# Optimization experiments

Hardware: AMD Instinct MI355X
Metric: run time of the kernel (lower is better)

## Reference

```python
import jax, jax.numpy as jnp
import numpy as np
import math

EPS_LN = 1e-5
SCALE = 16.0  # cosine_sim_scale


def layer_norm(x, g):
    mean = jnp.mean(x, axis=-1, keepdims=True)
    var = jnp.var(x, axis=-1, keepdims=True)  # biased, matches unbiased=False
    return (x - mean) * jax.lax.rsqrt(var + EPS_LN) * g


def l2norm(t):
    n = jnp.linalg.norm(t, axis=-1, keepdims=True)
    return t / jnp.maximum(n, 1e-12)


def setup_inputs() -> dict:
    key = jax.random.key(0)
    ks = jax.random.split(key, 4)
    b, n, dim, h, dh = 4, 2048, 1024, 8, 64
    inner = h * dh
    x = jax.random.normal(ks[0], (b, n, dim), dtype=jnp.float32)
    Wq = jax.random.normal(ks[1], (dim, inner), dtype=jnp.float32) * (dim ** -0.5)
    Wkv = jax.random.normal(ks[2], (dim, 2 * dh), dtype=jnp.float32) * (dim ** -0.5)
    Wout = jax.random.normal(ks[3], (inner, dim), dtype=jnp.float32) * (inner ** -0.5)
    norm_g = jnp.ones((dim,), dtype=jnp.float32)
    out_norm_g = jnp.ones((dim,), dtype=jnp.float32)
    return {"x": x, "norm_g": norm_g, "Wq": Wq, "Wkv": Wkv, "Wout": Wout,
            "out_norm_g": out_norm_g}


def reference(x, norm_g, Wq, Wkv, Wout, out_norm_g):
    b, n, dim = x.shape
    h = 8
    dh = Wkv.shape[-1] // 2
    xn = layer_norm(x, norm_g)
    q = xn @ Wq                      # [b, n, h*dh]
    kv = xn @ Wkv                    # [b, n, 2*dh]
    k, v = kv[..., :dh], kv[..., dh:]
    q = q.reshape(b, n, h, dh).transpose(0, 2, 1, 3)  # [b, h, n, dh]
    q = q * SCALE                    # cancelled by l2norm, kept for fidelity
    q = l2norm(q)
    k = l2norm(k)
    rs = math.sqrt(SCALE)
    q = q * rs
    k = k * rs
    sim = jnp.einsum('bhid,bjd->bhij', q, k)          # [b, h, n, n]
    attn = jax.nn.softmax(sim.astype(jnp.float32), axis=-1).astype(sim.dtype)
    out = jnp.einsum('bhij,bjd->bhid', attn, v)       # [b, h, n, dh]
    out = out.transpose(0, 2, 1, 3).reshape(b, n, h * dh)
    out = out @ Wout
    return layer_norm(out, out_norm_g)
```

## Files before the change

kernel.cpp:

```cpp
#include <hip/hip_runtime.h>
#include <hip/hip_bf16.h>

typedef __attribute__((ext_vector_type(8))) short short8;
typedef __attribute__((ext_vector_type(4))) float floatx4;

__device__ __forceinline__ float bf2f(ushort u) {
    return __uint_as_float(((unsigned int)u) << 16);
}
__device__ __forceinline__ ushort f2bf(float f) {
    unsigned int u = __float_as_uint(f);
    unsigned int r = (u + 0x7FFFu + ((u >> 16) & 1u)) >> 16;
    return (ushort)r;
}
__device__ __forceinline__ unsigned int pk2(float a, float b) {
    union { __hip_bfloat162 h; unsigned int u; } cv;
    cv.h = __float22bfloat162_rn(make_float2(a, b));
    return cv.u;
}
__device__ __forceinline__ float scrub(float v, float lim) {
    return fminf(fmaxf(v, -lim), lim);
}

__device__ __forceinline__ bool detect_bf16(const ushort* __restrict__ probe) {
    const int lane = threadIdx.x & 63;
    ushort u = probe[(lane & 31) * 2];
    int e = (u >> 7) & 0xFF;
    bool pl = (e >= 117) && (e <= 131) && (lane < 32);
    return __popcll(__ballot(pl)) >= 16;
}

__global__ __launch_bounds__(256) void ln1_kernel(const void* __restrict__ xin,
                                                  const void* __restrict__ gin,
                                                  ushort* __restrict__ out,
                                                  const ushort* __restrict__ probe) {
    const bool ib = detect_bf16(probe);
    const int row = blockIdx.x;
    const int tid = threadIdx.x;

    float v0, v1, v2, v3, g0, g1, g2, g3;
    if (ib) {
        uint2 u = *(const uint2*)((const ushort*)xin + (size_t)row * 1024 + tid * 4);
        v0 = bf2f((ushort)(u.x & 0xFFFF)); v1 = bf2f((ushort)(u.x >> 16));
        v2 = bf2f((ushort)(u.y & 0xFFFF)); v3 = bf2f((ushort)(u.y >> 16));
        uint2 gu = *(const uint2*)((const ushort*)gin + tid * 4);
        g0 = bf2f((ushort)(gu.x & 0xFFFF)); g1 = bf2f((ushort)(gu.x >> 16));
        g2 = bf2f((ushort)(gu.y & 0xFFFF)); g3 = bf2f((ushort)(gu.y >> 16));
    } else {
        float4 xv = *(const float4*)((const float*)xin + (size_t)row * 1024 + tid * 4);
        v0 = xv.x; v1 = xv.y; v2 = xv.z; v3 = xv.w;
        float4 gv = *(const float4*)((const float*)gin + tid * 4);
        g0 = gv.x; g1 = gv.y; g2 = gv.z; g3 = gv.w;
    }
    v0 = scrub(v0, 1e8f); v1 = scrub(v1, 1e8f); v2 = scrub(v2, 1e8f); v3 = scrub(v3, 1e8f);
    g0 = scrub(g0, 1e8f); g1 = scrub(g1, 1e8f); g2 = scrub(g2, 1e8f); g3 = scrub(g3, 1e8f);

    float s  = v0 + v1 + v2 + v3;
    float sq = v0 * v0 + v1 * v1 + v2 * v2 + v3 * v3;
    #pragma unroll
    for (int off = 1; off < 64; off <<= 1) {
        s  += __shfl_xor(s, off);
        sq += __shfl_xor(sq, off);
    }
    __shared__ float red[8];
    const int w = tid >> 6, lane = tid & 63;
    if (lane == 0) { red[w] = s; red[w + 4] = sq; }
    __syncthreads();
    float S  = red[0] + red[1] + red[2] + red[3];
    float SQ = red[4] + red[5] + red[6] + red[7];

    float mean = S * (1.0f / 1024.0f);
    float var  = SQ * (1.0f / 1024.0f) - mean * mean;
    float rstd = rsqrtf(fmaxf(var, 0.0f) + 1e-5f);

    uint2 ov;
    ov.x = pk2((v0 - mean) * rstd * g0, (v1 - mean) * rstd * g1);
    ov.y = pk2((v2 - mean) * rstd * g2, (v3 - mean) * rstd * g3);
    *(uint2*)(out + (size_t)row * 1024 + tid * 4) = ov;
}

__global__ __launch_bounds__(256) void ln2_kernel(const ushort* __restrict__ y,
                                                  const void* __restrict__ gin,
                                                  void* __restrict__ out,
                                                  const ushort* __restrict__ probe) {
    const bool ob = detect_bf16(probe);
    const int row = blockIdx.x;
    const int tid = threadIdx.x;

    uint2 u = *(const uint2*)(y + (size_t)row * 1024 + tid * 4);
    float v0 = scrub(bf2f((ushort)(u.x & 0xFFFF)), 1e8f);
    float v1 = scrub(bf2f((ushort)(u.x >> 16)),    1e8f);
    float v2 = scrub(bf2f((ushort)(u.y & 0xFFFF)), 1e8f);
    float v3 = scrub(bf2f((ushort)(u.y >> 16)),    1e8f);

    float g0, g1, g2, g3;
    if (ob) {
        uint2 gu = *(const uint2*)((const ushort*)gin + tid * 4);
        g0 = bf2f((ushort)(gu.x & 0xFFFF)); g1 = bf2f((ushort)(gu.x >> 16));
        g2 = bf2f((ushort)(gu.y & 0xFFFF)); g3 = bf2f((ushort)(gu.y >> 16));
    } else {
        float4 gv = *(const float4*)((const float*)gin + tid * 4);
        g0 = gv.x; g1 = gv.y; g2 = gv.z; g3 = gv.w;
    }
    g0 = scrub(g0, 1e8f); g1 = scrub(g1, 1e8f); g2 = scrub(g2, 1e8f); g3 = scrub(g3, 1e8f);

    float s  = v0 + v1 + v2 + v3;
    float sq = v0 * v0 + v1 * v1 + v2 * v2 + v3 * v3;
    #pragma unroll
    for (int off = 1; off < 64; off <<= 1) {
        s  += __shfl_xor(s, off);
        sq += __shfl_xor(sq, off);
    }
    __shared__ float red[8];
    const int w = tid >> 6, lane = tid & 63;
    if (lane == 0) { red[w] = s; red[w + 4] = sq; }
    __syncthreads();
    float S  = red[0] + red[1] + red[2] + red[3];
    float SQ = red[4] + red[5] + red[6] + red[7];

    float mean = S * (1.0f / 1024.0f);
    float var  = SQ * (1.0f / 1024.0f) - mean * mean;
    float rstd = rsqrtf(fmaxf(var, 0.0f) + 1e-5f);

    float o0 = (v0 - mean) * rstd * g0;
    float o1 = (v1 - mean) * rstd * g1;
    float o2 = (v2 - mean) * rstd * g2;
    float o3 = (v3 - mean) * rstd * g3;
    if (ob) {
        uint2 ov;
        ov.x = pk2(o0, o1);
        ov.y = pk2(o2, o3);
        *(uint2*)((ushort*)out + (size_t)row * 1024 + tid * 4) = ov;
    } else {
        *(float4*)((float*)out + (size_t)row * 1024 + tid * 4) = make_float4(o0, o1, o2, o3);
    }
}

__global__ __launch_bounds__(256) void transpose_kernel(const void* __restrict__ in,
                                                        ushort* __restrict__ out,
                                                        int in_rs, long long in_bs,
                                                        int out_rs, long long out_bs,
                                                        int force_bf16,
                                                        const ushort* __restrict__ probe) {
    const bool ib = force_bf16 ? true : detect_bf16(probe);
    __shared__ ushort tile[32][33];
    const int tx = threadIdx.x & 31, ty = threadIdx.x >> 5;

    #pragma unroll
    for (int rr = 0; rr < 32; rr += 8) {
        size_t idx = (size_t)blockIdx.z * in_bs + (size_t)(blockIdx.y * 32 + ty + rr) * in_rs
                   + blockIdx.x * 32 + tx;
        float v = ib ? bf2f(((const ushort*)in)[idx]) : ((const float*)in)[idx];
        tile[ty + rr][tx] = f2bf(scrub(v, 1e8f));
    }
    __syncthreads();
    ushort* op = out + (size_t)blockIdx.z * out_bs;
    #pragma unroll
    for (int rr = 0; rr < 32; rr += 8) {
        int r = blockIdx.x * 32 + ty + rr;
        int c = blockIdx.y * 32 + tx;
        op[(size_t)r * out_rs + c] = tile[tx][ty + rr];
    }
}

__global__ __launch_bounds__(256) void gemm_qkv(const ushort* __restrict__ A,
                                                const ushort* __restrict__ Bt,
                                                ushort* __restrict__ qb,
                                                ushort* __restrict__ kb,
                                                ushort* __restrict__ vt) {
    __shared__ ushort a_t[64][40];
    __shared__ ushort b_t[64][40];

    const int bx = blockIdx.x;
    const int n0 = bx * 64, m0 = blockIdx.y * 64;
    const int tid = threadIdx.x;
    const int w = tid >> 6, lane = tid & 63;
    const int fm = lane & 15, quad = lane >> 4;
    const int lrow = tid >> 2, lk = (tid & 3) * 8;
    const int K = 1024;

    const ushort* ag = A + (size_t)(m0 + lrow) * K + lk;
    const ushort* bg = Bt + (size_t)(n0 + lrow) * K + lk;

    floatx4 acc[4];
    floatx4 zero4 = {0.0f, 0.0f, 0.0f, 0.0f};
    #pragma unroll
    for (int nt = 0; nt < 4; nt++) acc[nt] = zero4;

    for (int k0 = 0; k0 < K; k0 += 32) {
        uint4 av = *(const uint4*)(ag + k0);
        uint4 bv = *(const uint4*)(bg + k0);
        __syncthreads();
        *(uint2*)&a_t[lrow][lk]     = make_uint2(av.x, av.y);
        *(uint2*)&a_t[lrow][lk + 4] = make_uint2(av.z, av.w);
        *(uint2*)&b_t[lrow][lk]     = make_uint2(bv.x, bv.y);
        *(uint2*)&b_t[lrow][lk + 4] = make_uint2(bv.z, bv.w);
        __syncthreads();

        union { uint2 u2[2]; short8 s8; } af;
        af.u2[0] = *(const uint2*)&a_t[w * 16 + fm][quad * 8];
        af.u2[1] = *(const uint2*)&a_t[w * 16 + fm][quad * 8 + 4];
        #pragma unroll
        for (int nt = 0; nt < 4; nt++) {
            union { uint2 u2[2]; short8 s8; } bf;
            bf.u2[0] = *(const uint2*)&b_t[nt * 16 + fm][quad * 8];
            bf.u2[1] = *(const uint2*)&b_t[nt * 16 + fm][quad * 8 + 4];
            acc[nt] = __builtin_amdgcn_mfma_f32_16x16x32_bf16(af.s8, bf.s8, acc[nt], 0, 0, 0);
        }
    }

    if (bx < 9) {
        float sc[4];
        #pragma unroll
        for (int r = 0; r < 4; r++) {
            float ss = acc[0][r] * acc[0][r] + acc[1][r] * acc[1][r]
                     + acc[2][r] * acc[2][r] + acc[3][r] * acc[3][r];
            ss += __shfl_xor(ss, 1);
            ss += __shfl_xor(ss, 2);
            ss += __shfl_xor(ss, 4);
            ss += __shfl_xor(ss, 8);
            sc[r] = 4.0f / fmaxf(sqrtf(ss), 1e-12f);
        }
        ushort* op;
        int rs;
        if (bx < 8) { op = qb + n0; rs = 512; }
        else        { op = kb;      rs = 64;  }
        #pragma unroll
        for (int nt = 0; nt < 4; nt++)
            #pragma unroll
            for (int r = 0; r < 4; r++)
                op[(size_t)(m0 + w * 16 + quad * 4 + r) * rs + nt * 16 + fm] =
                    f2bf(acc[nt][r] * sc[r]);
    } else {
        const int b = m0 >> 11;
        const int jb = (m0 & 2047) + w * 16 + quad * 4;
        ushort* vb = vt + (size_t)b * 64 * 2048 + jb;
        #pragma unroll
        for (int nt = 0; nt < 4; nt++) {
            uint2 pv;
            pv.x = pk2(acc[nt][0], acc[nt][1]);
            pv.y = pk2(acc[nt][2], acc[nt][3]);
            *(uint2*)(vb + (size_t)(nt * 16 + fm) * 2048) = pv;
        }
    }
}

__global__ __launch_bounds__(256) void gemm_bt(const ushort* __restrict__ A,
                                               const ushort* __restrict__ Bt,
                                               ushort* __restrict__ C,
                                               int M, int N, int K) {
    __shared__ ushort a_t[64][40];
    __shared__ ushort b_t[64][40];

    const int n0 = blockIdx.x * 64, m0 = blockIdx.y * 64;
    const int tid = threadIdx.x;
    const int w = tid >> 6, lane = tid & 63;
    const int fm = lane & 15, quad = lane >> 4;
    const int lrow = tid >> 2, lk = (tid & 3) * 8;

    const ushort* ag = A + (size_t)(m0 + lrow) * K + lk;
    const ushort* bg = Bt + (size_t)(n0 + lrow) * K + lk;

    floatx4 acc[4];
    floatx4 zero4 = {0.0f, 0.0f, 0.0f, 0.0f};
    #pragma unroll
    for (int nt = 0; nt < 4; nt++) acc[nt] = zero4;

    for (int k0 = 0; k0 < K; k0 += 32) {
        uint4 av = *(const uint4*)(ag + k0);
        uint4 bv = *(const uint4*)(bg + k0);
        __syncthreads();
        *(uint2*)&a_t[lrow][lk]     = make_uint2(av.x, av.y);
        *(uint2*)&a_t[lrow][lk + 4] = make_uint2(av.z, av.w);
        *(uint2*)&b_t[lrow][lk]     = make_uint2(bv.x, bv.y);
        *(uint2*)&b_t[lrow][lk + 4] = make_uint2(bv.z, bv.w);
        __syncthreads();

        union { uint2 u2[2]; short8 s8; } af;
        af.u2[0] = *(const uint2*)&a_t[w * 16 + fm][quad * 8];
        af.u2[1] = *(const uint2*)&a_t[w * 16 + fm][quad * 8 + 4];
        #pragma unroll
        for (int nt = 0; nt < 4; nt++) {
            union { uint2 u2[2]; short8 s8; } bf;
            bf.u2[0] = *(const uint2*)&b_t[nt * 16 + fm][quad * 8];
            bf.u2[1] = *(const uint2*)&b_t[nt * 16 + fm][quad * 8 + 4];
            acc[nt] = __builtin_amdgcn_mfma_f32_16x16x32_bf16(af.s8, bf.s8, acc[nt], 0, 0, 0);
        }
    }

    #pragma unroll
    for (int nt = 0; nt < 4; nt++)
        #pragma unroll
        for (int r = 0; r < 4; r++)
            C[(size_t)(m0 + w * 16 + quad * 4 + r) * N + n0 + nt * 16 + fm] = f2bf(acc[nt][r]);
}

__global__ __launch_bounds__(512, 4) void attn_kernel(const ushort* __restrict__ q,
                                                      const ushort* __restrict__ kb,
                                                      const ushort* __restrict__ vt,
                                                      ushort* __restrict__ out) {
    __shared__ ushort k_t[64][72];
    __shared__ ushort v_t[64][72];
    __shared__ ushort p_tile[8][16][72];

    const int i0 = blockIdx.x * 128;
    const int h = blockIdx.y, b = blockIdx.z;
    const int tid = threadIdx.x, w = tid >> 6, lane = tid & 63;
    const int fm = lane & 15, quad = lane >> 4;

    union U8 { uint4 u4; short8 s8; };

    const ushort* qbase = q + ((size_t)(b * 2048 + i0 + w * 16 + fm) * 512) + h * 64 + quad * 8;
    U8 qf0, qf1;
    qf0.u4 = *(const uint4*)qbase;
    qf1.u4 = *(const uint4*)(qbase + 32);

    floatx4 zero4 = {0.0f, 0.0f, 0.0f, 0.0f};
    floatx4 acc_o[4];
    #pragma unroll
    for (int od = 0; od < 4; od++) acc_o[od] = zero4;
    float lsum = 0.0f;

    const ushort* kbb = kb + (size_t)b * 2048 * 64;
    const ushort* vtb = vt + (size_t)b * 64 * 2048;

    const int srow = tid >> 3;
    const int sk = (tid & 7) * 8;

    for (int j0 = 0; j0 < 2048; j0 += 64) {
        uint4 ka = *(const uint4*)(kbb + (size_t)(j0 + srow) * 64 + sk);
        uint4 va = *(const uint4*)(vtb + (size_t)srow * 2048 + j0 + sk);
        __syncthreads();
        *(uint4*)&k_t[srow][sk] = ka;
        *(uint4*)&v_t[srow][sk] = va;
        __syncthreads();

        #pragma unroll
        for (int nt = 0; nt < 4; nt++) {
            U8 kb0, kb1;
            kb0.u4 = *(const uint4*)&k_t[nt * 16 + fm][quad * 8];
            kb1.u4 = *(const uint4*)&k_t[nt * 16 + fm][quad * 8 + 32];
            floatx4 st = zero4;
            st = __builtin_amdgcn_mfma_f32_16x16x32_bf16(kb0.s8, qf0.s8, st, 0, 0, 0);
            st = __builtin_amdgcn_mfma_f32_16x16x32_bf16(kb1.s8, qf1.s8, st, 0, 0, 0);
            float p0 = __expf(fminf(st[0], 16.0f) - 16.0f);
            float p1 = __expf(fminf(st[1], 16.0f) - 16.0f);
            float p2 = __expf(fminf(st[2], 16.0f) - 16.0f);
            float p3 = __expf(fminf(st[3], 16.0f) - 16.0f);
            lsum += (p0 + p1) + (p2 + p3);
            uint2 pkv;
            pkv.x = pk2(p0, p1);
            pkv.y = pk2(p2, p3);
            *(uint2*)&p_tile[w][fm][nt * 16 + quad * 4] = pkv;
        }

        U8 pb0, pb1;
        pb0.u4 = *(const uint4*)&p_tile[w][fm][quad * 8];
        pb1.u4 = *(const uint4*)&p_tile[w][fm][32 + quad * 8];

        #pragma unroll
        for (int od = 0; od < 4; od++) {
            U8 vb0, vb1;
            vb0.u4 = *(const uint4*)&v_t[od * 16 + fm][quad * 8];
            vb1.u4 = *(const uint4*)&v_t[od * 16 + fm][quad * 8 + 32];
            acc_o[od] = __builtin_amdgcn_mfma_f32_16x16x32_bf16(vb0.s8, pb0.s8, acc_o[od], 0, 0, 0);
            acc_o[od] = __builtin_amdgcn_mfma_f32_16x16x32_bf16(vb1.s8, pb1.s8, acc_o[od], 0, 0, 0);
        }
    }

    lsum += __shfl_xor(lsum, 16);
    lsum += __shfl_xor(lsum, 32);
    float li = 1.0f / fmaxf(lsum, 1e-30f);

    ushort* ob = out + (size_t)(b * 2048 + i0 + w * 16 + fm) * 512 + h * 64;
    #pragma unroll
    for (int od = 0; od < 4; od++) {
        uint2 ov;
        ov.x = pk2(acc_o[od][0] * li, acc_o[od][1] * li);
        ov.y = pk2(acc_o[od][2] * li, acc_o[od][3] * li);
        *(uint2*)(ob + od * 16 + quad * 4) = ov;
    }
}

extern "C" void kernel_launch(void* const* d_in, const int* in_sizes, int n_in,
                              void* d_out, int out_size, void* d_ws, size_t ws_size,
                              hipStream_t stream) {
    const void* x          = d_in[0];
    const void* norm_g     = d_in[1];
    const void* Wq         = d_in[2];
    const void* Wkv        = d_in[3];
    const void* Wout       = d_in[4];
    const void* out_norm_g = d_in[5];
    const ushort* probe = (const ushort*)d_in[0];
    ushort* ws = (ushort*)d_ws;

    const size_t M1 = 1024 * 1024 / 2;
    ushort* xn    = (ushort*)d_out;
    ushort* ao    = (ushort*)d_out;
    ushort* woT   = (ushort*)((char*)d_out + (8u << 20));
    ushort* qb    = ws;
    ushort* kb    = ws + 8 * M1;
    ushort* vt    = ws + 9 * M1;
    ushort* wcatT = ws + 11 * M1;
    ushort* y     = ws;

    transpose_kernel<<<dim3(16, 32, 1), 256, 0, stream>>>(Wq, wcatT, 512, 0, 1024, 0, 0, probe);
    transpose_kernel<<<dim3(4, 32, 1), 256, 0, stream>>>(Wkv, wcatT + (size_t)512 * 1024, 128, 0, 1024, 0, 0, probe);

    ln1_kernel<<<8192, 256, 0, stream>>>(x, norm_g, xn, probe);

    gemm_qkv<<<dim3(10, 128), 256, 0, stream>>>(xn, wcatT, qb, kb, vt);

    transpose_kernel<<<dim3(32, 16, 1), 256, 0, stream>>>(Wout, woT, 1024, 0, 512, 0, 0, probe);

    attn_kernel<<<dim3(16, 8, 4), 512, 0, stream>>>(qb, kb, vt, ao);

    gemm_bt<<<dim3(16, 128), 256, 0, stream>>>(ao, woT, y, 8192, 1024, 512);

    ln2_kernel<<<8192, 256, 0, stream>>>(y, out_norm_g, d_out, probe);
}
```

Baseline: 230.0 us.

## Give each attention wave two query tiles and fold weight transposes into kernels

```diff
diff --git a/kernel.cpp b/kernel.cpp
--- a/kernel.cpp
+++ b/kernel.cpp
@@ -29,14 +29,51 @@
     return __popcll(__ballot(pl)) >= 16;
 }
 
-__global__ __launch_bounds__(256) void ln1_kernel(const void* __restrict__ xin,
-                                                  const void* __restrict__ gin,
-                                                  ushort* __restrict__ out,
-                                                  const ushort* __restrict__ probe) {
+__device__ __forceinline__ void do_transpose(const void* __restrict__ in,
+                                             ushort* __restrict__ out,
+                                             int bx, int by, int in_rs, int out_rs,
+                                             bool ib, ushort* tile ) {
+    const int tx = threadIdx.x & 31, ty = threadIdx.x >> 5;
+    #pragma unroll
+    for (int rr = 0; rr < 32; rr += 8) {
+        size_t idx = (size_t)(by * 32 + ty + rr) * in_rs + bx * 32 + tx;
+        float v = ib ? bf2f(((const ushort*)in)[idx]) : ((const float*)in)[idx];
+        tile[(ty + rr) * 33 + tx] = f2bf(scrub(v, 1e8f));
+    }
+    __syncthreads();
+    #pragma unroll
+    for (int rr = 0; rr < 32; rr += 8) {
+        int r = bx * 32 + ty + rr;
+        int c = by * 32 + tx;
+        out[(size_t)r * out_rs + c] = tile[tx * 33 + (ty + rr)];
+    }
+}
+
+__global__ __launch_bounds__(256) void prep_kernel(const void* __restrict__ xin,
+                                                   const void* __restrict__ gin,
+                                                   const void* __restrict__ Wq,
+                                                   const void* __restrict__ Wkv,
+                                                   ushort* __restrict__ xn,
+                                                   ushort* __restrict__ wcatT,
+                                                   const ushort* __restrict__ probe) {
     const bool ib = detect_bf16(probe);
-    const int row = blockIdx.x;
+    const int id = blockIdx.x;
+    __shared__ ushort tile[32 * 33];
+    __shared__ float red[8];
+
+    if (id >= 8192) {
+        if (id < 8704) {
+            int t = id - 8192;
+            do_transpose(Wq, wcatT, t & 15, t >> 4, 512, 1024, ib, tile);
+        } else {
+            int t = id - 8704;
+            do_transpose(Wkv, wcatT + (size_t)512 * 1024, t & 3, t >> 2, 128, 1024, ib, tile);
+        }
+        return;
+    }
+
+    const int row = id;
     const int tid = threadIdx.x;
-
     float v0, v1, v2, v3, g0, g1, g2, g3;
     if (ib) {
         uint2 u = *(const uint2*)((const ushort*)xin + (size_t)row * 1024 + tid * 4);
@@ -61,7 +98,6 @@
         s  += __shfl_xor(s, off);
         sq += __shfl_xor(sq, off);
     }
-    __shared__ float red[8];
     const int w = tid >> 6, lane = tid & 63;
     if (lane == 0) { red[w] = s; red[w + 4] = sq; }
     __syncthreads();
@@ -75,7 +111,7 @@
     uint2 ov;
     ov.x = pk2((v0 - mean) * rstd * g0, (v1 - mean) * rstd * g1);
     ov.y = pk2((v2 - mean) * rstd * g2, (v3 - mean) * rstd * g3);
-    *(uint2*)(out + (size_t)row * 1024 + tid * 4) = ov;
+    *(uint2*)(xn + (size_t)row * 1024 + tid * 4) = ov;
 }
 
 __global__ __launch_bounds__(256) void ln2_kernel(const ushort* __restrict__ y,
@@ -135,33 +171,6 @@
     }
 }
 
-__global__ __launch_bounds__(256) void transpose_kernel(const void* __restrict__ in,
-                                                        ushort* __restrict__ out,
-                                                        int in_rs, long long in_bs,
-                                                        int out_rs, long long out_bs,
-                                                        int force_bf16,
-                                                        const ushort* __restrict__ probe) {
-    const bool ib = force_bf16 ? true : detect_bf16(probe);
-    __shared__ ushort tile[32][33];
-    const int tx = threadIdx.x & 31, ty = threadIdx.x >> 5;
-
-    #pragma unroll
-    for (int rr = 0; rr < 32; rr += 8) {
-        size_t idx = (size_t)blockIdx.z * in_bs + (size_t)(blockIdx.y * 32 + ty + rr) * in_rs
-                   + blockIdx.x * 32 + tx;
-        float v = ib ? bf2f(((const ushort*)in)[idx]) : ((const float*)in)[idx];
-        tile[ty + rr][tx] = f2bf(scrub(v, 1e8f));
-    }
-    __syncthreads();
-    ushort* op = out + (size_t)blockIdx.z * out_bs;
-    #pragma unroll
-    for (int rr = 0; rr < 32; rr += 8) {
-        int r = blockIdx.x * 32 + ty + rr;
-        int c = blockIdx.y * 32 + tx;
-        op[(size_t)r * out_rs + c] = tile[tx][ty + rr];
-    }
-}
-
 __global__ __launch_bounds__(256) void gemm_qkv(const ushort* __restrict__ A,
                                                 const ushort* __restrict__ Bt,
                                                 ushort* __restrict__ qb,
@@ -294,13 +303,23 @@
             C[(size_t)(m0 + w * 16 + quad * 4 + r) * N + n0 + nt * 16 + fm] = f2bf(acc[nt][r]);
 }
 
-__global__ __launch_bounds__(512, 4) void attn_kernel(const ushort* __restrict__ q,
+__global__ __launch_bounds__(256, 4) void attn_kernel(const ushort* __restrict__ q,
                                                       const ushort* __restrict__ kb,
                                                       const ushort* __restrict__ vt,
-                                                      ushort* __restrict__ out) {
+                                                      ushort* __restrict__ out,
+                                                      const void* __restrict__ Wout,
+                                                      ushort* __restrict__ woT,
+                                                      const ushort* __restrict__ probe) {
     __shared__ ushort k_t[64][72];
     __shared__ ushort v_t[64][72];
-    __shared__ ushort p_tile[8][16][72];
+    __shared__ ushort p_tile[4][32][72];
+
+    if (blockIdx.x >= 16) {
+        const bool ib = detect_bf16(probe);
+        int id = (blockIdx.x - 16) + 16 * (blockIdx.y + 8 * blockIdx.z);
+        do_transpose(Wout, woT, id & 31, id >> 5, 1024, 512, ib, &k_t[0][0]);
+        return;
+    }
 
     const int i0 = blockIdx.x * 128;
     const int h = blockIdx.y, b = blockIdx.z;
@@ -309,16 +328,19 @@
 
     union U8 { uint4 u4; short8 s8; };
 
-    const ushort* qbase = q + ((size_t)(b * 2048 + i0 + w * 16 + fm) * 512) + h * 64 + quad * 8;
-    U8 qf0, qf1;
-    qf0.u4 = *(const uint4*)qbase;
-    qf1.u4 = *(const uint4*)(qbase + 32);
+    const ushort* qbA = q + ((size_t)(b * 2048 + i0 + w * 32 + fm) * 512) + h * 64 + quad * 8;
+    const ushort* qbB = qbA + (size_t)16 * 512;
+    U8 qfA0, qfA1, qfB0, qfB1;
+    qfA0.u4 = *(const uint4*)qbA;
+    qfA1.u4 = *(const uint4*)(qbA + 32);
+    qfB0.u4 = *(const uint4*)qbB;
+    qfB1.u4 = *(const uint4*)(qbB + 32);
 
     floatx4 zero4 = {0.0f, 0.0f, 0.0f, 0.0f};
-    floatx4 acc_o[4];
-    #pragma unroll
-    for (int od = 0; od < 4; od++) acc_o[od] = zero4;
-    float lsum = 0.0f;
+    floatx4 accA[4], accB[4];
+    #pragma unroll
+    for (int od = 0; od < 4; od++) { accA[od] = zero4; accB[od] = zero4; }
+    float lsumA = 0.0f, lsumB = 0.0f;
 
     const ushort* kbb = kb + (size_t)b * 2048 * 64;
     const ushort* vtb = vt + (size_t)b * 64 * 2048;
@@ -327,57 +349,85 @@
     const int sk = (tid & 7) * 8;
 
     for (int j0 = 0; j0 < 2048; j0 += 64) {
-        uint4 ka = *(const uint4*)(kbb + (size_t)(j0 + srow) * 64 + sk);
-        uint4 va = *(const uint4*)(vtb + (size_t)srow * 2048 + j0 + sk);
-        __syncthreads();
-        *(uint4*)&k_t[srow][sk] = ka;
-        *(uint4*)&v_t[srow][sk] = va;
+        uint4 ka0 = *(const uint4*)(kbb + (size_t)(j0 + srow) * 64 + sk);
+        uint4 ka1 = *(const uint4*)(kbb + (size_t)(j0 + srow + 32) * 64 + sk);
+        uint4 va0 = *(const uint4*)(vtb + (size_t)srow * 2048 + j0 + sk);
+        uint4 va1 = *(const uint4*)(vtb + (size_t)(srow + 32) * 2048 + j0 + sk);
+        __syncthreads();
+        *(uint4*)&k_t[srow][sk]      = ka0;
+        *(uint4*)&k_t[srow + 32][sk] = ka1;
+        *(uint4*)&v_t[srow][sk]      = va0;
+        *(uint4*)&v_t[srow + 32][sk] = va1;
         __syncthreads();
 
         #pragma unroll
         for (int nt = 0; nt < 4; nt++) {
-            U8 kb0, kb1;
-            kb0.u4 = *(const uint4*)&k_t[nt * 16 + fm][quad * 8];
-            kb1.u4 = *(const uint4*)&k_t[nt * 16 + fm][quad * 8 + 32];
-            floatx4 st = zero4;
-            st = __builtin_amdgcn_mfma_f32_16x16x32_bf16(kb0.s8, qf0.s8, st, 0, 0, 0);
-            st = __builtin_amdgcn_mfma_f32_16x16x32_bf16(kb1.s8, qf1.s8, st, 0, 0, 0);
-            float p0 = __expf(fminf(st[0], 16.0f) - 16.0f);
-            float p1 = __expf(fminf(st[1], 16.0f) - 16.0f);
-            float p2 = __expf(fminf(st[2], 16.0f) - 16.0f);
-            float p3 = __expf(fminf(st[3], 16.0f) - 16.0f);
-            lsum += (p0 + p1) + (p2 + p3);
-            uint2 pkv;
-            pkv.x = pk2(p0, p1);
-            pkv.y = pk2(p2, p3);
-            *(uint2*)&p_tile[w][fm][nt * 16 + quad * 4] = pkv;
-        }
-
-        U8 pb0, pb1;
-        pb0.u4 = *(const uint4*)&p_tile[w][fm][quad * 8];
-        pb1.u4 = *(const uint4*)&p_tile[w][fm][32 + quad * 8];
+            U8 kf0, kf1;
+            kf0.u4 = *(const uint4*)&k_t[nt * 16 + fm][quad * 8];
+            kf1.u4 = *(const uint4*)&k_t[nt * 16 + fm][quad * 8 + 32];
+            floatx4 stA = zero4, stB = zero4;
+            stA = __builtin_amdgcn_mfma_f32_16x16x32_bf16(kf0.s8, qfA0.s8, stA, 0, 0, 0);
+            stA = __builtin_amdgcn_mfma_f32_16x16x32_bf16(kf1.s8, qfA1.s8, stA, 0, 0, 0);
+            stB = __builtin_amdgcn_mfma_f32_16x16x32_bf16(kf0.s8, qfB0.s8, stB, 0, 0, 0);
+            stB = __builtin_amdgcn_mfma_f32_16x16x32_bf16(kf1.s8, qfB1.s8, stB, 0, 0, 0);
+
+            float a0 = __expf(fminf(stA[0], 16.0f) - 16.0f);
+            float a1 = __expf(fminf(stA[1], 16.0f) - 16.0f);
+            float a2 = __expf(fminf(stA[2], 16.0f) - 16.0f);
+            float a3 = __expf(fminf(stA[3], 16.0f) - 16.0f);
+            lsumA += (a0 + a1) + (a2 + a3);
+            uint2 pa;
+            pa.x = pk2(a0, a1);
+            pa.y = pk2(a2, a3);
+            *(uint2*)&p_tile[w][fm][nt * 16 + quad * 4] = pa;
+
+            float b0 = __expf(fminf(stB[0], 16.0f) - 16.0f);
+            float b1 = __expf(fminf(stB[1], 16.0f) - 16.0f);
+            float b2 = __expf(fminf(stB[2], 16.0f) - 16.0f);
+            float b3 = __expf(fminf(stB[3], 16.0f) - 16.0f);
+            lsumB += (b0 + b1) + (b2 + b3);
+            uint2 pb;
+            pb.x = pk2(b0, b1);
+            pb.y = pk2(b2, b3);
+            *(uint2*)&p_tile[w][16 + fm][nt * 16 + quad * 4] = pb;
+        }
+
+        U8 pA0, pA1, pB0, pB1;
+        pA0.u4 = *(const uint4*)&p_tile[w][fm][quad * 8];
+        pA1.u4 = *(const uint4*)&p_tile[w][fm][32 + quad * 8];
+        pB0.u4 = *(const uint4*)&p_tile[w][16 + fm][quad * 8];
+        pB1.u4 = *(const uint4*)&p_tile[w][16 + fm][32 + quad * 8];
 
         #pragma unroll
         for (int od = 0; od < 4; od++) {
-            U8 vb0, vb1;
-            vb0.u4 = *(const uint4*)&v_t[od * 16 + fm][quad * 8];
-            vb1.u4 = *(const uint4*)&v_t[od * 16 + fm][quad * 8 + 32];
-            acc_o[od] = __builtin_amdgcn_mfma_f32_16x16x32_bf16(vb0.s8, pb0.s8, acc_o[od], 0, 0, 0);
-            acc_o[od] = __builtin_amdgcn_mfma_f32_16x16x32_bf16(vb1.s8, pb1.s8, acc_o[od], 0, 0, 0);
-        }
-    }
-
-    lsum += __shfl_xor(lsum, 16);
-    lsum += __shfl_xor(lsum, 32);
-    float li = 1.0f / fmaxf(lsum, 1e-30f);
-
-    ushort* ob = out + (size_t)(b * 2048 + i0 + w * 16 + fm) * 512 + h * 64;
+            U8 vf0, vf1;
+            vf0.u4 = *(const uint4*)&v_t[od * 16 + fm][quad * 8];
+            vf1.u4 = *(const uint4*)&v_t[od * 16 + fm][quad * 8 + 32];
+            accA[od] = __builtin_amdgcn_mfma_f32_16x16x32_bf16(vf0.s8, pA0.s8, accA[od], 0, 0, 0);
+            accA[od] = __builtin_amdgcn_mfma_f32_16x16x32_bf16(vf1.s8, pA1.s8, accA[od], 0, 0, 0);
+            accB[od] = __builtin_amdgcn_mfma_f32_16x16x32_bf16(vf0.s8, pB0.s8, accB[od], 0, 0, 0);
+            accB[od] = __builtin_amdgcn_mfma_f32_16x16x32_bf16(vf1.s8, pB1.s8, accB[od], 0, 0, 0);
+        }
+    }
+
+    lsumA += __shfl_xor(lsumA, 16);
+    lsumA += __shfl_xor(lsumA, 32);
+    lsumB += __shfl_xor(lsumB, 16);
+    lsumB += __shfl_xor(lsumB, 32);
+    float liA = 1.0f / fmaxf(lsumA, 1e-30f);
+    float liB = 1.0f / fmaxf(lsumB, 1e-30f);
+
+    ushort* obA = out + (size_t)(b * 2048 + i0 + w * 32 + fm) * 512 + h * 64;
+    ushort* obB = obA + (size_t)16 * 512;
     #pragma unroll
     for (int od = 0; od < 4; od++) {
-        uint2 ov;
-        ov.x = pk2(acc_o[od][0] * li, acc_o[od][1] * li);
-        ov.y = pk2(acc_o[od][2] * li, acc_o[od][3] * li);
-        *(uint2*)(ob + od * 16 + quad * 4) = ov;
+        uint2 ovA, ovB;
+        ovA.x = pk2(accA[od][0] * liA, accA[od][1] * liA);
+        ovA.y = pk2(accA[od][2] * liA, accA[od][3] * liA);
+        ovB.x = pk2(accB[od][0] * liB, accB[od][1] * liB);
+        ovB.y = pk2(accB[od][2] * liB, accB[od][3] * liB);
+        *(uint2*)(obA + od * 16 + quad * 4) = ovA;
+        *(uint2*)(obB + od * 16 + quad * 4) = ovB;
     }
 }
 
@@ -403,16 +453,11 @@
     ushort* wcatT = ws + 11 * M1;
     ushort* y     = ws;
 
-    transpose_kernel<<<dim3(16, 32, 1), 256, 0, stream>>>(Wq, wcatT, 512, 0, 1024, 0, 0, probe);
-    transpose_kernel<<<dim3(4, 32, 1), 256, 0, stream>>>(Wkv, wcatT + (size_t)512 * 1024, 128, 0, 1024, 0, 0, probe);
-
-    ln1_kernel<<<8192, 256, 0, stream>>>(x, norm_g, xn, probe);
+    prep_kernel<<<8832, 256, 0, stream>>>(x, norm_g, Wq, Wkv, xn, wcatT, probe);
 
     gemm_qkv<<<dim3(10, 128), 256, 0, stream>>>(xn, wcatT, qb, kb, vt);
 
-    transpose_kernel<<<dim3(32, 16, 1), 256, 0, stream>>>(Wout, woT, 1024, 0, 512, 0, 0, probe);
-
-    attn_kernel<<<dim3(16, 8, 4), 512, 0, stream>>>(qb, kb, vt, ao);
+    attn_kernel<<<dim3(32, 8, 4), 256, 0, stream>>>(qb, kb, vt, ao, Wout, woT, probe);
 
     gemm_bt<<<dim3(16, 128), 256, 0, stream>>>(ao, woT, y, 8192, 1024, 512);
 
```

Result: slower. 260.6 us (+13.3%).
